# Optimization experiments

Hardware: AMD Instinct MI355X
Metric: run time of the kernel (lower is better)

Reference implementation:

```python
import jax, jax.numpy as jnp
import numpy as np

H, D, RPE_DIM, LAYERS = 8, 64, 64, 3
GAMMA = 0.999  # fixed decay (use_decay=True, requires_grad=False)
EPS = 1e-8

def simple_rmsnorm(x):
    # SimpleRMSNorm: x / (||x||_2 * d^{-1/2} + eps), no learned scale
    rms = jnp.sqrt(jnp.sum(x * x, axis=-1, keepdims=True)) * (x.shape[-1] ** -0.5)
    return x / (rms + EPS)

def rpe_transform(idx, pos_proj_w, pos_proj_b, layer_ws, layer_bs, out_w, out_b):
    # idx: (n, 1) -> (H, n, D)
    x = idx @ pos_proj_w + pos_proj_b            # (n, RPE_DIM)
    for i in range(LAYERS):                       # residual=False -> sequential
        x = jax.nn.relu(simple_rmsnorm(x)) @ layer_ws[i] + layer_bs[i]
    x = jax.nn.relu(simple_rmsnorm(x)) @ out_w + out_b   # (n, H*D)
    n = x.shape[0]
    return x.reshape(n, H, D).transpose(1, 0, 2)  # (H, n, D)

def setup_inputs() -> dict:
    key = jax.random.key(0)
    ks = jax.random.split(key, 6)
    b, n = 8, 4096
    s = RPE_DIM ** -0.5
    return {
        "x": jax.random.normal(ks[0], (b, H, n, D), jnp.float32),
        "pos_proj_w": jax.random.normal(ks[1], (1, RPE_DIM), jnp.float32),
        "pos_proj_b": jnp.zeros((RPE_DIM,), jnp.float32),
        "layer_ws": jax.random.normal(ks[2], (LAYERS, RPE_DIM, RPE_DIM), jnp.float32) * s,
        "layer_bs": jnp.zeros((LAYERS, RPE_DIM), jnp.float32),
        "out_w": jax.random.normal(ks[3], (RPE_DIM, H * D), jnp.float32) * s,
        "out_b": jnp.zeros((H * D,), jnp.float32),
    }

def reference(x, pos_proj_w, pos_proj_b, layer_ws, layer_bs, out_w, out_b):
    b, h, n, d = x.shape
    _rpe = lambda idx: rpe_transform(idx, pos_proj_w, pos_proj_b, layer_ws, layer_bs, out_w, out_b)
    # relative-position kernel values (par_type=1: raw integer offsets)
    zero = _rpe(jnp.zeros((1, 1), x.dtype))                       # (H, 1, D)
    pos_idx = jnp.arange(1, n, dtype=x.dtype).reshape(n - 1, 1)   # 1..n-1
    pos = _rpe(pos_idx)                                           # (H, n-1, D)
    neg = _rpe(-pos_idx[::-1])                                    # -(n-1)..-1
    # fixed exponential decay gamma^|offset|
    coef = jnp.arange(1, n, dtype=x.dtype).reshape(1, n - 1, 1)
    gamma = jnp.full((h, 1, d), GAMMA, x.dtype) ** coef           # (H, n-1, D)
    pos = gamma * pos
    neg = gamma[:, ::-1, :] * neg
    # act_type='none' -> identity activation on a
    a = jnp.concatenate([zero, pos, zero, neg], axis=1)           # (H, 2n, D)
    # circular conv of length 2n realizes the Toeplitz matvec
    y = jnp.fft.rfft(x, n=2 * n, axis=-2)                         # (b,H,n+1?,D) complex
    v = jnp.fft.rfft(a, n=2 * n, axis=-2)[None]                   # (1,H,.,D)
    out = jnp.fft.irfft(v * y, n=2 * n, axis=-2)[:, :, :n, :]
    return out
```

## Files before the change

### kernel.cpp

```cpp
#include <hip/hip_runtime.h>
#include <math.h>

#define NF 8192

__device__ __forceinline__ int phys(int e) { return e ^ (((e >> 4) & 7) << 1); }

__device__ __forceinline__ float2 cmul(float2 a, float2 b) {
    return make_float2(a.x*b.x - a.y*b.y, a.x*b.y + a.y*b.x);
}
__device__ __forceinline__ float2 cmulc(float2 a, float2 b) {
    return make_float2(a.x*b.x + a.y*b.y, a.y*b.x - a.x*b.y);
}
__device__ __forceinline__ float2 cadd(float2 a, float2 b){ return make_float2(a.x+b.x, a.y+b.y); }
__device__ __forceinline__ float2 csub(float2 a, float2 b){ return make_float2(a.x-b.x, a.y-b.y); }
__device__ __forceinline__ float2 mnegi(float2 a){ return make_float2(a.y, -a.x); }
__device__ __forceinline__ float2 mposi(float2 a){ return make_float2(-a.y, a.x); }
#define RSQ2 0.70710678118654752f
__device__ __forceinline__ float2 mw81 (float2 a){ return make_float2( RSQ2*(a.x+a.y),  RSQ2*(a.y-a.x)); }
__device__ __forceinline__ float2 mw83 (float2 a){ return make_float2( RSQ2*(a.y-a.x), -RSQ2*(a.x+a.y)); }
__device__ __forceinline__ float2 mw81c(float2 a){ return make_float2( RSQ2*(a.x-a.y),  RSQ2*(a.x+a.y)); }
__device__ __forceinline__ float2 mw83c(float2 a){ return make_float2(-RSQ2*(a.x+a.y),  RSQ2*(a.x-a.y)); }

template<int M, int LM>
__device__ __forceinline__ void fwd8(float2* Z, const float2* __restrict__ tw, int tid) {
    #pragma unroll
    for (int q = 0; q < 4; ++q) {
        int beta = tid + q*256;
        int i    = beta & (M-1);
        int base = ((beta >> LM) << (LM+3)) + i;
        float2 v0 = Z[phys(base        )];
        float2 v1 = Z[phys(base + 1*M)];
        float2 v2 = Z[phys(base + 2*M)];
        float2 v3 = Z[phys(base + 3*M)];
        float2 v4 = Z[phys(base + 4*M)];
        float2 v5 = Z[phys(base + 5*M)];
        float2 v6 = Z[phys(base + 6*M)];
        float2 v7 = Z[phys(base + 7*M)];
        float2 t;
        t = csub(v0, v4); v0 = cadd(v0, v4); v4 = t;
        t = csub(v1, v5); v1 = cadd(v1, v5); v5 = mw81(t);
        t = csub(v2, v6); v2 = cadd(v2, v6); v6 = mnegi(t);
        t = csub(v3, v7); v3 = cadd(v3, v7); v7 = mw83(t);
        t = csub(v0, v2); v0 = cadd(v0, v2); v2 = t;
        t = csub(v1, v3); v1 = cadd(v1, v3); v3 = mnegi(t);
        t = csub(v4, v6); v4 = cadd(v4, v6); v6 = t;
        t = csub(v5, v7); v5 = cadd(v5, v7); v7 = mnegi(t);
        t = csub(v0, v1); v0 = cadd(v0, v1); v1 = t;
        t = csub(v2, v3); v2 = cadd(v2, v3); v3 = t;
        t = csub(v4, v5); v4 = cadd(v4, v5); v5 = t;
        t = csub(v6, v7); v6 = cadd(v6, v7); v7 = t;
        int ts = (NF >> (LM+3)) * i;
        Z[phys(base        )] = v0;
        Z[phys(base + 4*M)] = cmul(v1, tw[ts*4]);
        Z[phys(base + 2*M)] = cmul(v2, tw[ts*2]);
        Z[phys(base + 6*M)] = cmul(v3, tw[ts*6]);
        Z[phys(base + 1*M)] = cmul(v4, tw[ts  ]);
        Z[phys(base + 5*M)] = cmul(v5, tw[ts*5]);
        Z[phys(base + 3*M)] = cmul(v6, tw[ts*3]);
        Z[phys(base + 7*M)] = cmul(v7, tw[ts*7]);
    }
}

template<int M, int LM>
__device__ __forceinline__ void inv8(float2* Z, const float2* __restrict__ tw, int tid) {
    #pragma unroll
    for (int q = 0; q < 4; ++q) {
        int beta = tid + q*256;
        int i    = beta & (M-1);
        int base = ((beta >> LM) << (LM+3)) + i;
        int ts   = (NF >> (LM+3)) * i;
        float2 v0 = Z[phys(base        )];
        float2 v1 = cmulc(Z[phys(base + 4*M)], tw[ts*4]);
        float2 v2 = cmulc(Z[phys(base + 2*M)], tw[ts*2]);
        float2 v3 = cmulc(Z[phys(base + 6*M)], tw[ts*6]);
        float2 v4 = cmulc(Z[phys(base + 1*M)], tw[ts  ]);
        float2 v5 = cmulc(Z[phys(base + 5*M)], tw[ts*5]);
        float2 v6 = cmulc(Z[phys(base + 3*M)], tw[ts*3]);
        float2 v7 = cmulc(Z[phys(base + 7*M)], tw[ts*7]);
        float2 t;
        t = csub(v0, v1); v0 = cadd(v0, v1); v1 = t;
        t = csub(v2, v3); v2 = cadd(v2, v3); v3 = t;
        t = csub(v4, v5); v4 = cadd(v4, v5); v5 = t;
        t = csub(v6, v7); v6 = cadd(v6, v7); v7 = t;
        t = v2;        v2 = csub(v0, t); v0 = cadd(v0, t);
        t = mposi(v3); v3 = csub(v1, t); v1 = cadd(v1, t);
        t = v6;        v6 = csub(v4, t); v4 = cadd(v4, t);
        t = mposi(v7); v7 = csub(v5, t); v5 = cadd(v5, t);
        t = v4;        v4 = csub(v0, t); v0 = cadd(v0, t);
        t = mw81c(v5); v5 = csub(v1, t); v1 = cadd(v1, t);
        t = mposi(v6); v6 = csub(v2, t); v2 = cadd(v2, t);
        t = mw83c(v7); v7 = csub(v3, t); v3 = cadd(v3, t);
        Z[phys(base        )] = v0;
        Z[phys(base + 1*M)] = v1;
        Z[phys(base + 2*M)] = v2;
        Z[phys(base + 3*M)] = v3;
        Z[phys(base + 4*M)] = v4;
        Z[phys(base + 5*M)] = v5;
        Z[phys(base + 6*M)] = v6;
        Z[phys(base + 7*M)] = v7;
    }
}

__device__ __forceinline__ void fwd2(float2* Z, int tid) {
    #pragma unroll
    for (int q = 0; q < 16; ++q) {
        int beta = tid + q*256;
        int pe = phys(2*beta);
        float4 z = *reinterpret_cast<float4*>(&Z[pe]);
        float2 u = make_float2(z.x, z.y), w = make_float2(z.z, z.w);
        float2 p = cadd(u, w), r = csub(u, w);
        *reinterpret_cast<float4*>(&Z[pe]) = make_float4(p.x, p.y, r.x, r.y);
    }
}

__device__ __forceinline__ void fused_mul(float2* Z, const float4* __restrict__ A4, int tid) {
    #pragma unroll
    for (int q = 0; q < 16; ++q) {
        int beta = tid + q*256;
        int pe = phys(2*beta);
        float4 z = *reinterpret_cast<float4*>(&Z[pe]);
        float2 u = make_float2(z.x, z.y), w = make_float2(z.z, z.w);
        float2 p = cadd(u, w), r = csub(u, w);
        float4 a = A4[beta];
        p = cmul(p, make_float2(a.x, a.y));
        r = cmul(r, make_float2(a.z, a.w));
        float2 o0 = cadd(p, r), o1 = csub(p, r);
        *reinterpret_cast<float4*>(&Z[pe]) = make_float4(o0.x, o0.y, o1.x, o1.y);
    }
}

__global__ void twiddle_kernel(float2* __restrict__ tw) {
    int j = blockIdx.x * 256 + threadIdx.x;
    double ang = -6.283185307179586476925286766559 * (double)j / 8192.0;
    tw[j] = make_float2((float)cos(ang), (float)sin(ang));
}

__global__ __launch_bounds__(256) void rpe_kernel(
    const float* __restrict__ pw,  const float* __restrict__ pb,
    const float* __restrict__ lws, const float* __restrict__ lbs,
    const float* __restrict__ ow,  const float* __restrict__ ob,
    float* __restrict__ a_buf)
{
    __shared__ float sW[3][64][64];
    __shared__ float sAct[4][4][64];
    __shared__ float sTmp[4][64];
    __shared__ float sB[3][64];
    __shared__ float sPW[64], sPB[64];
    int tid = threadIdx.x;
    for (int idx = tid; idx < 3*64*64; idx += 256) ((float*)sW)[idx] = lws[idx];
    if (tid < 3*64) ((float*)sB)[tid] = lbs[tid];
    if (tid < 64) { sPW[tid] = pw[tid]; sPB[tid] = pb[tid]; }
    __syncthreads();

    int wave = tid >> 6, lane = tid & 63;
    int ebase = blockIdx.x * 16 + wave * 4;
    float dec[4];
    #pragma unroll
    for (int s = 0; s < 4; ++s) {
        int e = ebase + s;
        float p = (e == 4096) ? 0.f : ((e < 4096) ? (float)e : (float)(e - 8192));
        int m = (e < 4096) ? e : (8192 - e);
        if (e == 4096) m = 0;
        dec[s] = exp2f(-0.0014434309482562475f * (float)m);
        float xv = fmaf(p, sPW[lane], sPB[lane]);
        for (int L = 0; L < 3; ++L) {
            float ss = xv * xv;
            #pragma unroll
            for (int o = 1; o < 64; o <<= 1) ss += __shfl_xor(ss, o);
            float act = xv / (sqrtf(ss) * 0.125f + 1e-8f);
            act = fmaxf(act, 0.f);
            sTmp[wave][lane] = act;
            __syncthreads();
            float y0 = sB[L][lane], y1 = 0.f;
            #pragma unroll
            for (int k = 0; k < 64; k += 2) {
                y0 = fmaf(sTmp[wave][k],   sW[L][k][lane],   y0);
                y1 = fmaf(sTmp[wave][k+1], sW[L][k+1][lane], y1);
            }
            __syncthreads();
            xv = y0 + y1;
        }
        float ss = xv * xv;
        #pragma unroll
        for (int o = 1; o < 64; o <<= 1) ss += __shfl_xor(ss, o);
        float act = xv / (sqrtf(ss) * 0.125f + 1e-8f);
        sAct[wave][s][lane] = fmaxf(act, 0.f);
    }
    auto& sWo = sW[0];
    for (int qq = 0; qq < 8; ++qq) {
        __syncthreads();
        for (int idx = tid; idx < 4096; idx += 256)
            sWo[idx >> 6][idx & 63] = ow[(size_t)(idx >> 6)*512 + qq*64 + (idx & 63)];
        __syncthreads();
        #pragma unroll
        for (int s = 0; s < 4; ++s) {
            float y0 = ob[qq*64 + lane], y1 = 0.f, y2 = 0.f, y3 = 0.f;
            #pragma unroll
            for (int k = 0; k < 64; k += 4) {
                y0 = fmaf(sAct[wave][s][k],   sWo[k  ][lane], y0);
                y1 = fmaf(sAct[wave][s][k+1], sWo[k+1][lane], y1);
                y2 = fmaf(sAct[wave][s][k+2], sWo[k+2][lane], y2);
                y3 = fmaf(sAct[wave][s][k+3], sWo[k+3][lane], y3);
            }
            int e = ebase + s;
            a_buf[(size_t)(qq*64 + lane)*NF + e] = (y0+y1+y2+y3) * dec[s];
        }
    }
}

__global__ __launch_bounds__(256, 2) void afft_kernel(
    const float* __restrict__ a_buf, const float2* __restrict__ tw,
    float2* __restrict__ Afft)
{
    __shared__ float2 Z[NF];
    int cc = blockIdx.x, tid = threadIdx.x;
    const float* col = a_buf + (size_t)cc * NF;
    #pragma unroll
    for (int j = 0; j < 32; ++j) { int e = tid + j*256; Z[phys(e)] = make_float2(col[e], 0.f); }
    __syncthreads();
    fwd8<1024,10>(Z, tw, tid); __syncthreads();
    fwd8<128, 7>(Z, tw, tid);  __syncthreads();
    fwd8<16,  4>(Z, tw, tid);  __syncthreads();
    fwd8<2,   1>(Z, tw, tid);  __syncthreads();
    fwd2(Z, tid);              __syncthreads();
    float2* oc = Afft + (size_t)cc * NF;
    #pragma unroll
    for (int j = 0; j < 32; ++j) { int e = tid + j*256; oc[e] = Z[phys(e)]; }
}

__global__ __launch_bounds__(256, 2) void conv_kernel(
    const float* __restrict__ x, const float2* __restrict__ tw,
    const float2* __restrict__ Afft, float* __restrict__ out)
{
    __shared__ float2 Z[NF];
    int blk = blockIdx.x;
    int c = blk & 7, r = blk >> 3;
    int d  = ((c & 1) << 5) | (r & 31);
    int h  = (((r >> 5) & 3) << 1) | ((c >> 1) & 1);
    int bp = (((r >> 7) & 1) << 1) | ((c >> 2) & 1);
    int tid = threadIdx.x;
    size_t base0 = ((size_t)((bp*2 + 0)*8 + h) * 4096) * 64 + d;
    size_t base1 = ((size_t)((bp*2 + 1)*8 + h) * 4096) * 64 + d;
    #pragma unroll
    for (int j = 0; j < 16; ++j) {
        int t = tid + j*256;
        float re = x[base0 + (size_t)t*64];
        float im = x[base1 + (size_t)t*64];
        Z[phys(t)]        = make_float2(re, im);
        Z[phys(t + 4096)] = make_float2(0.f, 0.f);
    }
    __syncthreads();
    fwd8<1024,10>(Z, tw, tid); __syncthreads();
    fwd8<128, 7>(Z, tw, tid);  __syncthreads();
    fwd8<16,  4>(Z, tw, tid);  __syncthreads();
    fwd8<2,   1>(Z, tw, tid);  __syncthreads();
    const float4* A4 = reinterpret_cast<const float4*>(Afft + (size_t)(h*64 + d)*NF);
    fused_mul(Z, A4, tid);     __syncthreads();
    inv8<2,   1>(Z, tw, tid);  __syncthreads();
    inv8<16,  4>(Z, tw, tid);  __syncthreads();
    inv8<128, 7>(Z, tw, tid);  __syncthreads();
    inv8<1024,10>(Z, tw, tid); __syncthreads();
    const float sc = 1.0f/8192.0f;
    #pragma unroll
    for (int j = 0; j < 16; ++j) {
        int t = tid + j*256;
        float2 v = Z[phys(t)];
        out[base0 + (size_t)t*64] = v.x * sc;
        out[base1 + (size_t)t*64] = v.y * sc;
    }
}

extern "C" void kernel_launch(void* const* d_in, const int* in_sizes, int n_in,
                              void* d_out, int out_size, void* d_ws, size_t ws_size,
                              hipStream_t stream) {
    const float* x   = (const float*)d_in[0];
    const float* pw  = (const float*)d_in[1];
    const float* pb  = (const float*)d_in[2];
    const float* lws = (const float*)d_in[3];
    const float* lbs = (const float*)d_in[4];
    const float* ow  = (const float*)d_in[5];
    const float* ob  = (const float*)d_in[6];
    float* out = (float*)d_out;
    char* ws = (char*)d_ws;
    float2* tw    = (float2*)ws;
    float*  a_buf = (float*)(ws + 65536);
    float2* Afft  = (float2*)(ws + 65536 + (size_t)512*NF*4);

    twiddle_kernel<<<32, 256, 0, stream>>>(tw);
    rpe_kernel<<<512, 256, 0, stream>>>(pw, pb, lws, lbs, ow, ob, a_buf);
    afft_kernel<<<512, 256, 0, stream>>>(a_buf, tw, Afft);
    conv_kernel<<<2048, 256, 0, stream>>>(x, tw, Afft, out);
}
```

Measured before the change: 503.1 us.

## Fuse FFT edge stages into global load/store and use 512-thread blocks

The FFT kernels now run the first radix-8 stage directly from global loads and the last inverse stage directly into global stores, which removes two shared-memory passes and their barriers. In the conv kernel the zero-padded half is exploited to skip half the first butterfly. The final radix-16 forward stage, the spectrum multiply and the first inverse radix-16 stage are fused in registers using swizzled float4 LDS accesses. Blocks grow to 512 threads with fewer items per thread, and the RPE kernel processes one position per wave across 2048 blocks. The cost is higher register pressure per thread and strided global loads feeding straight into the butterfly.

```diff
diff --git a/kernel.cpp b/kernel.cpp
--- a/kernel.cpp
+++ b/kernel.cpp
@@ -21,11 +21,49 @@
 __device__ __forceinline__ float2 mw81c(float2 a){ return make_float2( RSQ2*(a.x-a.y),  RSQ2*(a.x+a.y)); }
 __device__ __forceinline__ float2 mw83c(float2 a){ return make_float2(-RSQ2*(a.x+a.y),  RSQ2*(a.x-a.y)); }
 
+#define C16_1 0.92387953251128674f
+#define S16_1 0.38268343236508978f
+#define C16_2 0.70710678118654752f
+
+__device__ __forceinline__ void dif8_core(float2& v0, float2& v1, float2& v2, float2& v3,
+                                          float2& v4, float2& v5, float2& v6, float2& v7) {
+    float2 t;
+    t = csub(v0, v4); v0 = cadd(v0, v4); v4 = t;
+    t = csub(v1, v5); v1 = cadd(v1, v5); v5 = mw81(t);
+    t = csub(v2, v6); v2 = cadd(v2, v6); v6 = mnegi(t);
+    t = csub(v3, v7); v3 = cadd(v3, v7); v7 = mw83(t);
+    t = csub(v0, v2); v0 = cadd(v0, v2); v2 = t;
+    t = csub(v1, v3); v1 = cadd(v1, v3); v3 = mnegi(t);
+    t = csub(v4, v6); v4 = cadd(v4, v6); v6 = t;
+    t = csub(v5, v7); v5 = cadd(v5, v7); v7 = mnegi(t);
+    t = csub(v0, v1); v0 = cadd(v0, v1); v1 = t;
+    t = csub(v2, v3); v2 = cadd(v2, v3); v3 = t;
+    t = csub(v4, v5); v4 = cadd(v4, v5); v5 = t;
+    t = csub(v6, v7); v6 = cadd(v6, v7); v7 = t;
+}
+
+__device__ __forceinline__ void dit8_core(float2& v0, float2& v1, float2& v2, float2& v3,
+                                          float2& v4, float2& v5, float2& v6, float2& v7) {
+    float2 t;
+    t = csub(v0, v1); v0 = cadd(v0, v1); v1 = t;
+    t = csub(v2, v3); v2 = cadd(v2, v3); v3 = t;
+    t = csub(v4, v5); v4 = cadd(v4, v5); v5 = t;
+    t = csub(v6, v7); v6 = cadd(v6, v7); v7 = t;
+    t = v2;        v2 = csub(v0, t); v0 = cadd(v0, t);
+    t = mposi(v3); v3 = csub(v1, t); v1 = cadd(v1, t);
+    t = v6;        v6 = csub(v4, t); v4 = cadd(v4, t);
+    t = mposi(v7); v7 = csub(v5, t); v5 = cadd(v5, t);
+    t = v4;        v4 = csub(v0, t); v0 = cadd(v0, t);
+    t = mw81c(v5); v5 = csub(v1, t); v1 = cadd(v1, t);
+    t = mposi(v6); v6 = csub(v2, t); v2 = cadd(v2, t);
+    t = mw83c(v7); v7 = csub(v3, t); v3 = cadd(v3, t);
+}
+
 template<int M, int LM>
-__device__ __forceinline__ void fwd8(float2* Z, const float2* __restrict__ tw, int tid) {
-    #pragma unroll
-    for (int q = 0; q < 4; ++q) {
-        int beta = tid + q*256;
+__device__ __forceinline__ void fwd8_lds(float2* Z, const float2* __restrict__ tw, int tid) {
+    #pragma unroll
+    for (int q = 0; q < 2; ++q) {
+        int beta = tid + q*512;
         int i    = beta & (M-1);
         int base = ((beta >> LM) << (LM+3)) + i;
         float2 v0 = Z[phys(base        )];
@@ -36,19 +74,7 @@
         float2 v5 = Z[phys(base + 5*M)];
         float2 v6 = Z[phys(base + 6*M)];
         float2 v7 = Z[phys(base + 7*M)];
-        float2 t;
-        t = csub(v0, v4); v0 = cadd(v0, v4); v4 = t;
-        t = csub(v1, v5); v1 = cadd(v1, v5); v5 = mw81(t);
-        t = csub(v2, v6); v2 = cadd(v2, v6); v6 = mnegi(t);
-        t = csub(v3, v7); v3 = cadd(v3, v7); v7 = mw83(t);
-        t = csub(v0, v2); v0 = cadd(v0, v2); v2 = t;
-        t = csub(v1, v3); v1 = cadd(v1, v3); v3 = mnegi(t);
-        t = csub(v4, v6); v4 = cadd(v4, v6); v6 = t;
-        t = csub(v5, v7); v5 = cadd(v5, v7); v7 = mnegi(t);
-        t = csub(v0, v1); v0 = cadd(v0, v1); v1 = t;
-        t = csub(v2, v3); v2 = cadd(v2, v3); v3 = t;
-        t = csub(v4, v5); v4 = cadd(v4, v5); v5 = t;
-        t = csub(v6, v7); v6 = cadd(v6, v7); v7 = t;
+        dif8_core(v0,v1,v2,v3,v4,v5,v6,v7);
         int ts = (NF >> (LM+3)) * i;
         Z[phys(base        )] = v0;
         Z[phys(base + 4*M)] = cmul(v1, tw[ts*4]);
@@ -62,10 +88,10 @@
 }
 
 template<int M, int LM>
-__device__ __forceinline__ void inv8(float2* Z, const float2* __restrict__ tw, int tid) {
-    #pragma unroll
-    for (int q = 0; q < 4; ++q) {
-        int beta = tid + q*256;
+__device__ __forceinline__ void inv8_lds(float2* Z, const float2* __restrict__ tw, int tid) {
+    #pragma unroll
+    for (int q = 0; q < 2; ++q) {
+        int beta = tid + q*512;
         int i    = beta & (M-1);
         int base = ((beta >> LM) << (LM+3)) + i;
         int ts   = (NF >> (LM+3)) * i;
@@ -77,6 +103,273 @@
         float2 v5 = cmulc(Z[phys(base + 5*M)], tw[ts*5]);
         float2 v6 = cmulc(Z[phys(base + 3*M)], tw[ts*3]);
         float2 v7 = cmulc(Z[phys(base + 7*M)], tw[ts*7]);
+        dit8_core(v0,v1,v2,v3,v4,v5,v6,v7);
+        Z[phys(base        )] = v0;
+        Z[phys(base + 1*M)] = v1;
+        Z[phys(base + 2*M)] = v2;
+        Z[phys(base + 3*M)] = v3;
+        Z[phys(base + 4*M)] = v4;
+        Z[phys(base + 5*M)] = v5;
+        Z[phys(base + 6*M)] = v6;
+        Z[phys(base + 7*M)] = v7;
+    }
+}
+
+__global__ void twiddle_kernel(float2* __restrict__ tw) {
+    int j = blockIdx.x * 256 + threadIdx.x;
+    double ang = -6.283185307179586476925286766559 * (double)j / 8192.0;
+    tw[j] = make_float2((float)cos(ang), (float)sin(ang));
+}
+
+__global__ __launch_bounds__(256) void rpe_kernel(
+    const float* __restrict__ pw,  const float* __restrict__ pb,
+    const float* __restrict__ lws, const float* __restrict__ lbs,
+    const float* __restrict__ ow,  const float* __restrict__ ob,
+    float* __restrict__ a_buf)
+{
+    __shared__ float sW[3][64][64];
+    __shared__ float sB[3][64];
+    __shared__ float sPW[64], sPB[64];
+    __shared__ float sAct[4][64];
+    int tid = threadIdx.x;
+    for (int idx = tid; idx < 3*64*64; idx += 256) ((float*)sW)[idx] = lws[idx];
+    if (tid < 3*64) ((float*)sB)[tid] = lbs[tid];
+    if (tid < 64) { sPW[tid] = pw[tid]; sPB[tid] = pb[tid]; }
+    __syncthreads();
+
+    int wave = tid >> 6, lane = tid & 63;
+    int e = blockIdx.x * 4 + wave;
+    float p = (e == 4096) ? 0.f : ((e < 4096) ? (float)e : (float)(e - 8192));
+    int m = (e < 4096) ? e : (8192 - e);
+    if (e == 4096) m = 0;
+    float dec = exp2f(-0.0014434309482562475f * (float)m);
+
+    float xv = fmaf(p, sPW[lane], sPB[lane]);
+    for (int L = 0; L < 3; ++L) {
+        float ss = xv * xv;
+        #pragma unroll
+        for (int o = 1; o < 64; o <<= 1) ss += __shfl_xor(ss, o);
+        float act = fmaxf(xv / (sqrtf(ss) * 0.125f + 1e-8f), 0.f);
+        sAct[wave][lane] = act;
+        __syncthreads();
+        float y0 = sB[L][lane], y1 = 0.f;
+        #pragma unroll
+        for (int k = 0; k < 64; k += 2) {
+            y0 = fmaf(sAct[wave][k],   sW[L][k][lane],   y0);
+            y1 = fmaf(sAct[wave][k+1], sW[L][k+1][lane], y1);
+        }
+        __syncthreads();
+        xv = y0 + y1;
+    }
+    {
+        float ss = xv * xv;
+        #pragma unroll
+        for (int o = 1; o < 64; o <<= 1) ss += __shfl_xor(ss, o);
+        sAct[wave][lane] = fmaxf(xv / (sqrtf(ss) * 0.125f + 1e-8f), 0.f);
+    }
+    auto& sWo = sW[0];
+    float res[8];
+    for (int qq = 0; qq < 8; ++qq) {
+        __syncthreads();
+        for (int idx = tid; idx < 4096; idx += 256)
+            ((float*)sWo)[idx] = ow[(size_t)(idx >> 6)*512 + qq*64 + (idx & 63)];
+        __syncthreads();
+        float y0 = ob[qq*64 + lane], y1 = 0.f, y2 = 0.f, y3 = 0.f;
+        #pragma unroll
+        for (int k = 0; k < 64; k += 4) {
+            y0 = fmaf(sAct[wave][k],   sWo[k  ][lane], y0);
+            y1 = fmaf(sAct[wave][k+1], sWo[k+1][lane], y1);
+            y2 = fmaf(sAct[wave][k+2], sWo[k+2][lane], y2);
+            y3 = fmaf(sAct[wave][k+3], sWo[k+3][lane], y3);
+        }
+        res[qq] = (y0+y1+y2+y3) * dec;
+    }
+    #pragma unroll
+    for (int qq = 0; qq < 8; ++qq)
+        a_buf[(size_t)(qq*64 + lane)*NF + e] = res[qq];
+}
+
+__global__ __launch_bounds__(512, 4) void afft_kernel(
+    const float* __restrict__ a_buf, const float2* __restrict__ tw,
+    float2* __restrict__ Afft)
+{
+    __shared__ __align__(16) float2 Z[NF];
+    int cc = blockIdx.x, tid = threadIdx.x;
+    const float* col = a_buf + (size_t)cc * NF;
+    #pragma unroll
+    for (int q = 0; q < 2; ++q) {
+        int i = tid + q*512;
+        float2 v0 = make_float2(col[i       ], 0.f);
+        float2 v1 = make_float2(col[i + 1024], 0.f);
+        float2 v2 = make_float2(col[i + 2048], 0.f);
+        float2 v3 = make_float2(col[i + 3072], 0.f);
+        float2 v4 = make_float2(col[i + 4096], 0.f);
+        float2 v5 = make_float2(col[i + 5120], 0.f);
+        float2 v6 = make_float2(col[i + 6144], 0.f);
+        float2 v7 = make_float2(col[i + 7168], 0.f);
+        dif8_core(v0,v1,v2,v3,v4,v5,v6,v7);
+        int ts = i;
+        Z[phys(i        )] = v0;
+        Z[phys(i + 4096)] = cmul(v1, tw[ts*4]);
+        Z[phys(i + 2048)] = cmul(v2, tw[ts*2]);
+        Z[phys(i + 6144)] = cmul(v3, tw[ts*6]);
+        Z[phys(i + 1024)] = cmul(v4, tw[ts  ]);
+        Z[phys(i + 5120)] = cmul(v5, tw[ts*5]);
+        Z[phys(i + 3072)] = cmul(v6, tw[ts*3]);
+        Z[phys(i + 7168)] = cmul(v7, tw[ts*7]);
+    }
+    __syncthreads();
+    fwd8_lds<128, 7>(Z, tw, tid);  __syncthreads();
+    fwd8_lds<16,  4>(Z, tw, tid);  __syncthreads();
+    {
+        int c = tid, sw4 = c & 7;
+        float4* Z4 = reinterpret_cast<float4*>(Z);
+        float4* oc4 = reinterpret_cast<float4*>(Afft + (size_t)cc * NF);
+        float2 z[16];
+        #pragma unroll
+        for (int j = 0; j < 8; ++j) {
+            float4 wv = Z4[c*8 + (j ^ sw4)];
+            z[2*j]   = make_float2(wv.x, wv.y);
+            z[2*j+1] = make_float2(wv.z, wv.w);
+        }
+        dif8_core(z[0],z[2],z[4],z[6],z[8],z[10],z[12],z[14]);
+        dif8_core(z[1],z[3],z[5],z[7],z[9],z[11],z[13],z[15]);
+        #define A4K(k, ZE, ZO, WR, WI) { \
+            float2 w = make_float2((WR)*(ZO).x - (WI)*(ZO).y, (WR)*(ZO).y + (WI)*(ZO).x); \
+            float2 pp = cadd(ZE, w), rr = csub(ZE, w); \
+            oc4[c*8 + (k)] = make_float4(pp.x, pp.y, rr.x, rr.y); }
+        { float2 pp = cadd(z[0], z[1]), rr = csub(z[0], z[1]);
+          oc4[c*8 + 0] = make_float4(pp.x, pp.y, rr.x, rr.y); }
+        A4K(1, z[8],  z[9],   C16_1, -S16_1)
+        A4K(2, z[4],  z[5],   C16_2, -C16_2)
+        A4K(3, z[12], z[13],  S16_1, -C16_1)
+        { float2 w = mnegi(z[3]);
+          float2 pp = cadd(z[2], w), rr = csub(z[2], w);
+          oc4[c*8 + 4] = make_float4(pp.x, pp.y, rr.x, rr.y); }
+        A4K(5, z[10], z[11], -S16_1, -C16_1)
+        A4K(6, z[6],  z[7],  -C16_2, -C16_2)
+        A4K(7, z[14], z[15], -C16_1, -S16_1)
+        #undef A4K
+    }
+}
+
+__global__ __launch_bounds__(512, 4) void conv_kernel(
+    const float* __restrict__ x, const float2* __restrict__ tw,
+    const float2* __restrict__ Afft, float* __restrict__ out)
+{
+    __shared__ __align__(16) float2 Z[NF];
+    int blk = blockIdx.x;
+    int c8 = blk & 7, r = blk >> 3;
+    int d  = ((c8 & 1) << 5) | (r & 31);
+    int h  = (((r >> 5) & 3) << 1) | ((c8 >> 1) & 1);
+    int bp = (((r >> 7) & 1) << 1) | ((c8 >> 2) & 1);
+    int tid = threadIdx.x;
+    size_t base0 = ((size_t)((bp*2 + 0)*8 + h) * 4096) * 64 + d;
+    size_t base1 = ((size_t)((bp*2 + 1)*8 + h) * 4096) * 64 + d;
+
+    #pragma unroll
+    for (int q = 0; q < 2; ++q) {
+        int i = tid + q*512;
+        float2 v0 = make_float2(x[base0 + (size_t)(i       )*64], x[base1 + (size_t)(i       )*64]);
+        float2 v1 = make_float2(x[base0 + (size_t)(i + 1024)*64], x[base1 + (size_t)(i + 1024)*64]);
+        float2 v2 = make_float2(x[base0 + (size_t)(i + 2048)*64], x[base1 + (size_t)(i + 2048)*64]);
+        float2 v3 = make_float2(x[base0 + (size_t)(i + 3072)*64], x[base1 + (size_t)(i + 3072)*64]);
+        float2 v4 = v0;
+        float2 v5 = mw81(v1);
+        float2 v6 = mnegi(v2);
+        float2 v7 = mw83(v3);
+        float2 t;
+        t = csub(v0, v2); v0 = cadd(v0, v2); v2 = t;
+        t = csub(v1, v3); v1 = cadd(v1, v3); v3 = mnegi(t);
+        t = csub(v4, v6); v4 = cadd(v4, v6); v6 = t;
+        t = csub(v5, v7); v5 = cadd(v5, v7); v7 = mnegi(t);
+        t = csub(v0, v1); v0 = cadd(v0, v1); v1 = t;
+        t = csub(v2, v3); v2 = cadd(v2, v3); v3 = t;
+        t = csub(v4, v5); v4 = cadd(v4, v5); v5 = t;
+        t = csub(v6, v7); v6 = cadd(v6, v7); v7 = t;
+        int ts = i;
+        Z[phys(i        )] = v0;
+        Z[phys(i + 4096)] = cmul(v1, tw[ts*4]);
+        Z[phys(i + 2048)] = cmul(v2, tw[ts*2]);
+        Z[phys(i + 6144)] = cmul(v3, tw[ts*6]);
+        Z[phys(i + 1024)] = cmul(v4, tw[ts  ]);
+        Z[phys(i + 5120)] = cmul(v5, tw[ts*5]);
+        Z[phys(i + 3072)] = cmul(v6, tw[ts*3]);
+        Z[phys(i + 7168)] = cmul(v7, tw[ts*7]);
+    }
+    __syncthreads();
+    fwd8_lds<128, 7>(Z, tw, tid);  __syncthreads();
+    fwd8_lds<16,  4>(Z, tw, tid);  __syncthreads();
+
+    {
+        int c = tid, sw4 = c & 7;
+        float4* Z4 = reinterpret_cast<float4*>(Z);
+        const float4* A4 = reinterpret_cast<const float4*>(Afft + (size_t)(h*64 + d)*NF);
+        float2 z[16];
+        #pragma unroll
+        for (int j = 0; j < 8; ++j) {
+            float4 wv = Z4[c*8 + (j ^ sw4)];
+            z[2*j]   = make_float2(wv.x, wv.y);
+            z[2*j+1] = make_float2(wv.z, wv.w);
+        }
+        dif8_core(z[0],z[2],z[4],z[6],z[8],z[10],z[12],z[14]);
+        dif8_core(z[1],z[3],z[5],z[7],z[9],z[11],z[13],z[15]);
+        #define P4K(k, ZE, ZO, WR, WI) { \
+            float2 w = make_float2((WR)*(ZO).x - (WI)*(ZO).y, (WR)*(ZO).y + (WI)*(ZO).x); \
+            float2 pp = cadd(ZE, w), rr = csub(ZE, w); \
+            float4 av = A4[c*8 + (k)]; \
+            pp = cmul(pp, make_float2(av.x, av.y)); \
+            rr = cmul(rr, make_float2(av.z, av.w)); \
+            ZE = cadd(pp, rr); \
+            ZO = csub(pp, rr); }
+        { float2 pp = cadd(z[0], z[1]), rr = csub(z[0], z[1]);
+          float4 av = A4[c*8 + 0];
+          pp = cmul(pp, make_float2(av.x, av.y));
+          rr = cmul(rr, make_float2(av.z, av.w));
+          z[0] = cadd(pp, rr); z[1] = csub(pp, rr); }
+        P4K(1, z[8],  z[9],   C16_1, -S16_1)
+        P4K(2, z[4],  z[5],   C16_2, -C16_2)
+        P4K(3, z[12], z[13],  S16_1, -C16_1)
+        { float2 w = mnegi(z[3]);
+          float2 pp = cadd(z[2], w), rr = csub(z[2], w);
+          float4 av = A4[c*8 + 4];
+          pp = cmul(pp, make_float2(av.x, av.y));
+          rr = cmul(rr, make_float2(av.z, av.w));
+          z[2] = cadd(pp, rr); z[3] = csub(pp, rr); }
+        P4K(5, z[10], z[11], -S16_1, -C16_1)
+        P4K(6, z[6],  z[7],  -C16_2, -C16_2)
+        P4K(7, z[14], z[15], -C16_1, -S16_1)
+        #undef P4K
+        z[3]  = mposi(z[3]);
+        z[5]  = cmul(z[5],  make_float2( C16_2,  C16_2));
+        z[7]  = cmul(z[7],  make_float2(-C16_2,  C16_2));
+        z[9]  = cmul(z[9],  make_float2( C16_1,  S16_1));
+        z[11] = cmul(z[11], make_float2(-S16_1,  C16_1));
+        z[13] = cmul(z[13], make_float2( S16_1,  C16_1));
+        z[15] = cmul(z[15], make_float2(-C16_1,  S16_1));
+        dit8_core(z[0],z[2],z[4],z[6],z[8],z[10],z[12],z[14]);
+        dit8_core(z[1],z[3],z[5],z[7],z[9],z[11],z[13],z[15]);
+        #pragma unroll
+        for (int j = 0; j < 8; ++j)
+            Z4[c*8 + (j ^ sw4)] = make_float4(z[2*j].x, z[2*j].y, z[2*j+1].x, z[2*j+1].y);
+    }
+    __syncthreads();
+    inv8_lds<16,  4>(Z, tw, tid);  __syncthreads();
+    inv8_lds<128, 7>(Z, tw, tid);  __syncthreads();
+
+    const float sc = 1.0f/8192.0f;
+    #pragma unroll
+    for (int q = 0; q < 2; ++q) {
+        int i = tid + q*512;
+        int ts = i;
+        float2 v0 = Z[phys(i        )];
+        float2 v1 = cmulc(Z[phys(i + 4096)], tw[ts*4]);
+        float2 v2 = cmulc(Z[phys(i + 2048)], tw[ts*2]);
+        float2 v3 = cmulc(Z[phys(i + 6144)], tw[ts*6]);
+        float2 v4 = cmulc(Z[phys(i + 1024)], tw[ts  ]);
+        float2 v5 = cmulc(Z[phys(i + 5120)], tw[ts*5]);
+        float2 v6 = cmulc(Z[phys(i + 3072)], tw[ts*3]);
+        float2 v7 = cmulc(Z[phys(i + 7168)], tw[ts*7]);
         float2 t;
         t = csub(v0, v1); v0 = cadd(v0, v1); v1 = t;
         t = csub(v2, v3); v2 = cadd(v2, v3); v3 = t;
@@ -86,187 +379,18 @@
         t = mposi(v3); v3 = csub(v1, t); v1 = cadd(v1, t);
         t = v6;        v6 = csub(v4, t); v4 = cadd(v4, t);
         t = mposi(v7); v7 = csub(v5, t); v5 = cadd(v5, t);
-        t = v4;        v4 = csub(v0, t); v0 = cadd(v0, t);
-        t = mw81c(v5); v5 = csub(v1, t); v1 = cadd(v1, t);
-        t = mposi(v6); v6 = csub(v2, t); v2 = cadd(v2, t);
-        t = mw83c(v7); v7 = csub(v3, t); v3 = cadd(v3, t);
-        Z[phys(base        )] = v0;
-        Z[phys(base + 1*M)] = v1;
-        Z[phys(base + 2*M)] = v2;
-        Z[phys(base + 3*M)] = v3;
-        Z[phys(base + 4*M)] = v4;
-        Z[phys(base + 5*M)] = v5;
-        Z[phys(base + 6*M)] = v6;
-        Z[phys(base + 7*M)] = v7;
-    }
-}
-
-__device__ __forceinline__ void fwd2(float2* Z, int tid) {
-    #pragma unroll
-    for (int q = 0; q < 16; ++q) {
-        int beta = tid + q*256;
-        int pe = phys(2*beta);
-        float4 z = *reinterpret_cast<float4*>(&Z[pe]);
-        float2 u = make_float2(z.x, z.y), w = make_float2(z.z, z.w);
-        float2 p = cadd(u, w), r = csub(u, w);
-        *reinterpret_cast<float4*>(&Z[pe]) = make_float4(p.x, p.y, r.x, r.y);
-    }
-}
-
-__device__ __forceinline__ void fused_mul(float2* Z, const float4* __restrict__ A4, int tid) {
-    #pragma unroll
-    for (int q = 0; q < 16; ++q) {
-        int beta = tid + q*256;
-        int pe = phys(2*beta);
-        float4 z = *reinterpret_cast<float4*>(&Z[pe]);
-        float2 u = make_float2(z.x, z.y), w = make_float2(z.z, z.w);
-        float2 p = cadd(u, w), r = csub(u, w);
-        float4 a = A4[beta];
-        p = cmul(p, make_float2(a.x, a.y));
-        r = cmul(r, make_float2(a.z, a.w));
-        float2 o0 = cadd(p, r), o1 = csub(p, r);
-        *reinterpret_cast<float4*>(&Z[pe]) = make_float4(o0.x, o0.y, o1.x, o1.y);
-    }
-}
-
-__global__ void twiddle_kernel(float2* __restrict__ tw) {
-    int j = blockIdx.x * 256 + threadIdx.x;
-    double ang = -6.283185307179586476925286766559 * (double)j / 8192.0;
-    tw[j] = make_float2((float)cos(ang), (float)sin(ang));
-}
-
-__global__ __launch_bounds__(256) void rpe_kernel(
-    const float* __restrict__ pw,  const float* __restrict__ pb,
-    const float* __restrict__ lws, const float* __restrict__ lbs,
-    const float* __restrict__ ow,  const float* __restrict__ ob,
-    float* __restrict__ a_buf)
-{
-    __shared__ float sW[3][64][64];
-    __shared__ float sAct[4][4][64];
-    __shared__ float sTmp[4][64];
-    __shared__ float sB[3][64];
-    __shared__ float sPW[64], sPB[64];
-    int tid = threadIdx.x;
-    for (int idx = tid; idx < 3*64*64; idx += 256) ((float*)sW)[idx] = lws[idx];
-    if (tid < 3*64) ((float*)sB)[tid] = lbs[tid];
-    if (tid < 64) { sPW[tid] = pw[tid]; sPB[tid] = pb[tid]; }
-    __syncthreads();
-
-    int wave = tid >> 6, lane = tid & 63;
-    int ebase = blockIdx.x * 16 + wave * 4;
-    float dec[4];
-    #pragma unroll
-    for (int s = 0; s < 4; ++s) {
-        int e = ebase + s;
-        float p = (e == 4096) ? 0.f : ((e < 4096) ? (float)e : (float)(e - 8192));
-        int m = (e < 4096) ? e : (8192 - e);
-        if (e == 4096) m = 0;
-        dec[s] = exp2f(-0.0014434309482562475f * (float)m);
-        float xv = fmaf(p, sPW[lane], sPB[lane]);
-        for (int L = 0; L < 3; ++L) {
-            float ss = xv * xv;
-            #pragma unroll
-            for (int o = 1; o < 64; o <<= 1) ss += __shfl_xor(ss, o);
-            float act = xv / (sqrtf(ss) * 0.125f + 1e-8f);
-            act = fmaxf(act, 0.f);
-            sTmp[wave][lane] = act;
-            __syncthreads();
-            float y0 = sB[L][lane], y1 = 0.f;
-            #pragma unroll
-            for (int k = 0; k < 64; k += 2) {
-                y0 = fmaf(sTmp[wave][k],   sW[L][k][lane],   y0);
-                y1 = fmaf(sTmp[wave][k+1], sW[L][k+1][lane], y1);
-            }
-            __syncthreads();
-            xv = y0 + y1;
-        }
-        float ss = xv * xv;
-        #pragma unroll
-        for (int o = 1; o < 64; o <<= 1) ss += __shfl_xor(ss, o);
-        float act = xv / (sqrtf(ss) * 0.125f + 1e-8f);
-        sAct[wave][s][lane] = fmaxf(act, 0.f);
-    }
-    auto& sWo = sW[0];
-    for (int qq = 0; qq < 8; ++qq) {
-        __syncthreads();
-        for (int idx = tid; idx < 4096; idx += 256)
-            sWo[idx >> 6][idx & 63] = ow[(size_t)(idx >> 6)*512 + qq*64 + (idx & 63)];
-        __syncthreads();
-        #pragma unroll
-        for (int s = 0; s < 4; ++s) {
-            float y0 = ob[qq*64 + lane], y1 = 0.f, y2 = 0.f, y3 = 0.f;
-            #pragma unroll
-            for (int k = 0; k < 64; k += 4) {
-                y0 = fmaf(sAct[wave][s][k],   sWo[k  ][lane], y0);
-                y1 = fmaf(sAct[wave][s][k+1], sWo[k+1][lane], y1);
-                y2 = fmaf(sAct[wave][s][k+2], sWo[k+2][lane], y2);
-                y3 = fmaf(sAct[wave][s][k+3], sWo[k+3][lane], y3);
-            }
-            int e = ebase + s;
-            a_buf[(size_t)(qq*64 + lane)*NF + e] = (y0+y1+y2+y3) * dec[s];
-        }
-    }
-}
-
-__global__ __launch_bounds__(256, 2) void afft_kernel(
-    const float* __restrict__ a_buf, const float2* __restrict__ tw,
-    float2* __restrict__ Afft)
-{
-    __shared__ float2 Z[NF];
-    int cc = blockIdx.x, tid = threadIdx.x;
-    const float* col = a_buf + (size_t)cc * NF;
-    #pragma unroll
-    for (int j = 0; j < 32; ++j) { int e = tid + j*256; Z[phys(e)] = make_float2(col[e], 0.f); }
-    __syncthreads();
-    fwd8<1024,10>(Z, tw, tid); __syncthreads();
-    fwd8<128, 7>(Z, tw, tid);  __syncthreads();
-    fwd8<16,  4>(Z, tw, tid);  __syncthreads();
-    fwd8<2,   1>(Z, tw, tid);  __syncthreads();
-    fwd2(Z, tid);              __syncthreads();
-    float2* oc = Afft + (size_t)cc * NF;
-    #pragma unroll
-    for (int j = 0; j < 32; ++j) { int e = tid + j*256; oc[e] = Z[phys(e)]; }
-}
-
-__global__ __launch_bounds__(256, 2) void conv_kernel(
-    const float* __restrict__ x, const float2* __restrict__ tw,
-    const float2* __restrict__ Afft, float* __restrict__ out)
-{
-    __shared__ float2 Z[NF];
-    int blk = blockIdx.x;
-    int c = blk & 7, r = blk >> 3;
-    int d  = ((c & 1) << 5) | (r & 31);
-    int h  = (((r >> 5) & 3) << 1) | ((c >> 1) & 1);
-    int bp = (((r >> 7) & 1) << 1) | ((c >> 2) & 1);
-    int tid = threadIdx.x;
-    size_t base0 = ((size_t)((bp*2 + 0)*8 + h) * 4096) * 64 + d;
-    size_t base1 = ((size_t)((bp*2 + 1)*8 + h) * 4096) * 64 + d;
-    #pragma unroll
-    for (int j = 0; j < 16; ++j) {
-        int t = tid + j*256;
-        float re = x[base0 + (size_t)t*64];
-        float im = x[base1 + (size_t)t*64];
-        Z[phys(t)]        = make_float2(re, im);
-        Z[phys(t + 4096)] = make_float2(0.f, 0.f);
-    }
-    __syncthreads();
-    fwd8<1024,10>(Z, tw, tid); __syncthreads();
-    fwd8<128, 7>(Z, tw, tid);  __syncthreads();
-    fwd8<16,  4>(Z, tw, tid);  __syncthreads();
-    fwd8<2,   1>(Z, tw, tid);  __syncthreads();
-    const float4* A4 = reinterpret_cast<const float4*>(Afft + (size_t)(h*64 + d)*NF);
-    fused_mul(Z, A4, tid);     __syncthreads();
-    inv8<2,   1>(Z, tw, tid);  __syncthreads();
-    inv8<16,  4>(Z, tw, tid);  __syncthreads();
-    inv8<128, 7>(Z, tw, tid);  __syncthreads();
-    inv8<1024,10>(Z, tw, tid); __syncthreads();
-    const float sc = 1.0f/8192.0f;
-    #pragma unroll
-    for (int j = 0; j < 16; ++j) {
-        int t = tid + j*256;
-        float2 v = Z[phys(t)];
-        out[base0 + (size_t)t*64] = v.x * sc;
-        out[base1 + (size_t)t*64] = v.y * sc;
+        v0 = cadd(v0, v4);
+        v1 = cadd(v1, mw81c(v5));
+        v2 = cadd(v2, mposi(v6));
+        v3 = cadd(v3, mw83c(v7));
+        out[base0 + (size_t)(i       )*64] = v0.x * sc;
+        out[base1 + (size_t)(i       )*64] = v0.y * sc;
+        out[base0 + (size_t)(i + 1024)*64] = v1.x * sc;
+        out[base1 + (size_t)(i + 1024)*64] = v1.y * sc;
+        out[base0 + (size_t)(i + 2048)*64] = v2.x * sc;
+        out[base1 + (size_t)(i + 2048)*64] = v2.y * sc;
+        out[base0 + (size_t)(i + 3072)*64] = v3.x * sc;
+        out[base1 + (size_t)(i + 3072)*64] = v3.y * sc;
     }
 }
 
@@ -287,7 +411,7 @@
     float2* Afft  = (float2*)(ws + 65536 + (size_t)512*NF*4);
 
     twiddle_kernel<<<32, 256, 0, stream>>>(tw);
-    rpe_kernel<<<512, 256, 0, stream>>>(pw, pb, lws, lbs, ow, ob, a_buf);
-    afft_kernel<<<512, 256, 0, stream>>>(a_buf, tw, Afft);
-    conv_kernel<<<2048, 256, 0, stream>>>(x, tw, Afft, out);
-}
+    rpe_kernel<<<2048, 256, 0, stream>>>(pw, pb, lws, lbs, ow, ob, a_buf);
+    afft_kernel<<<512, 512, 0, stream>>>(a_buf, tw, Afft);
+    conv_kernel<<<2048, 512, 0, stream>>>(x, tw, Afft, out);
+}
```

Result: slower. 586.5 us (+16.6%).
